# Kernel tuning notes

Measured on AMD Instinct MI355X. Metric: run time of the kernel, lower is better.

The kernel has to match this reference:

```python
import math
import jax, jax.numpy as jnp
import numpy as np

B, L, D, H = 2, 2048, 1024, 16
HD = D // H  # 64

def setup_inputs() -> dict:
    key = jax.random.key(0)
    k1, k2, k3 = jax.random.split(key, 3)
    x = jax.random.normal(k1, (B, L, D), dtype=jnp.float32)
    Wqkv = jax.random.normal(k2, (3 * D, D), dtype=jnp.float32) * (1.0 / math.sqrt(D))
    Wo = jax.random.normal(k3, (D, D), dtype=jnp.float32) * (1.0 / math.sqrt(D))
    return {"x": x, "Wqkv": Wqkv, "Wo": Wo}

def reference(x, Wqkv, Wo):
    # QKV projection (torch Linear: y = x @ W.T), then split
    qkv = jnp.einsum('bld,ed->ble', x, Wqkv)  # [B, L, 3D]
    q, k, v = jnp.split(qkv, 3, axis=-1)
    # [B, H, L, HD]
    q = q.reshape(B, L, H, HD).transpose(0, 2, 1, 3)
    k = k.reshape(B, L, H, HD).transpose(0, 2, 1, 3)
    v = v.reshape(B, L, H, HD).transpose(0, 2, 1, 3)
    # scores; causal mask applied before the 1/sqrt(d) scale (as in source;
    # -inf is unchanged by scaling so math matches scale-then-mask)
    scores = jnp.einsum('bhqd,bhkd->bhqk', q, k)
    causal = jnp.tril(jnp.ones((L, L), dtype=bool))
    scores = jnp.where(causal, scores, -jnp.inf)
    attn = jax.nn.softmax(scores / math.sqrt(HD), axis=-1)
    out = jnp.einsum('bhqk,bhkd->bhqd', attn, v)  # [B, H, L, HD]
    out = out.transpose(0, 2, 1, 3).reshape(B, L, D)
    # output projection (dropout is identity in eval / p=0)
    return jnp.einsum('bld,ed->ble', out, Wo)
```

## Files before the change

### kernel.cpp

```cpp
#include <hip/hip_runtime.h>
#include <hip/hip_bf16.h>
#include <cstdint>
#include <cstddef>

#define B_SZ 2
#define L_SEQ 2048
#define DM 1024
#define NH 16
#define HDIM 64
#define BL (B_SZ * L_SEQ)
#define QKV_N (3 * DM)

typedef __attribute__((ext_vector_type(4))) float f32x4;
typedef __attribute__((ext_vector_type(16))) float f32x16;
typedef __attribute__((ext_vector_type(8))) short bf16x8;
typedef __attribute__((ext_vector_type(4))) unsigned int u32x4;
typedef unsigned short u16;
typedef __attribute__((ext_vector_type(4))) unsigned short u16x4;

__device__ __forceinline__ float bf2f(u16 u) {
  union { unsigned int i; float f; } c; c.i = ((unsigned int)u) << 16; return c.f;
}
__device__ __forceinline__ u16 f2bf(float f) {
  union { float f; unsigned int i; } c; c.f = f;
  unsigned int r = c.i + 0x7fffu + ((c.i >> 16) & 1u);
  return (u16)(r >> 16);
}

__device__ __forceinline__ void gload_lds16(const void* g, void* l) {
  __builtin_amdgcn_global_load_lds(
      (const __attribute__((address_space(1))) void*)g,
      (__attribute__((address_space(3))) void*)l, 16, 0, 0);
}

__device__ __forceinline__ f32x16 mfma32(bf16x8 a, bf16x8 b, f32x16 c) {
  return __builtin_amdgcn_mfma_f32_32x32x16_bf16(a, b, c, 0, 0, 0);
}

__device__ __forceinline__ unsigned cvtpk(float lo, float hi) {
  unsigned r;
  asm("v_cvt_pk_bf16_f32 %0, %1, %2" : "=v"(r) : "v"(lo), "v"(hi));
  return r;
}
__device__ __forceinline__ void plswap(unsigned& a, unsigned& b) {
  asm("v_permlane32_swap_b32 %0, %1" : "+v"(a), "+v"(b));
}

template <int BASE>
__device__ __forceinline__ bf16x8 pack_bfrag(const f32x16& v) {
  unsigned a  = cvtpk(v[BASE + 0], v[BASE + 1]);
  unsigned a2 = cvtpk(v[BASE + 2], v[BASE + 3]);
  unsigned b  = cvtpk(v[BASE + 4], v[BASE + 5]);
  unsigned b2 = cvtpk(v[BASE + 6], v[BASE + 7]);
  plswap(a, b);
  plswap(a2, b2);
  u32x4 fw; fw[0] = a; fw[1] = a2; fw[2] = b; fw[3] = b2;
  return __builtin_bit_cast(bf16x8, fw);
}

__global__ __launch_bounds__(256) void cvt_f32_bf16(const float* __restrict__ in,
                                                    u16* __restrict__ out, int n4) {
  int i = blockIdx.x * blockDim.x + threadIdx.x;
  const int stride = gridDim.x * blockDim.x;
  for (; i < n4; i += stride) {
    float4 v = ((const float4*)in)[i];
    u16x4 o;
    o[0] = f2bf(v.x); o[1] = f2bf(v.y); o[2] = f2bf(v.z); o[3] = f2bf(v.w);
    ((u16x4*)out)[i] = o;
  }
}

template <bool BF16_OUT>
__global__ __launch_bounds__(256) void gemm_bt(
    const u16* __restrict__ A, const u16* __restrict__ B,
    void* __restrict__ Cv, int M, int N, int K) {
  __shared__ u16 As[128 * 32];
  __shared__ u16 Bs[128 * 32];
  const int tid = threadIdx.x;
  const int lane = tid & 63, w = tid >> 6;
  const int lr = lane & 15, lg = lane >> 4;
  const int wr = w >> 1, wc = w & 1;
  const int bm = blockIdx.y * 128, bn = blockIdx.x * 128;

  f32x4 acc[4][4] = {};

  const int l4 = lane >> 2;
  const int csw = ((lane & 3) ^ ((lane >> 3) & 3)) * 8;
  const size_t aoff0 = (size_t)(bm + (w * 2 + 0) * 16 + l4) * K + csw;
  const size_t aoff1 = (size_t)(bm + (w * 2 + 1) * 16 + l4) * K + csw;
  const size_t boff0 = (size_t)(bn + (w * 2 + 0) * 16 + l4) * K + csw;
  const size_t boff1 = (size_t)(bn + (w * 2 + 1) * 16 + l4) * K + csw;
  u16* As0 = As + (w * 2 + 0) * 512;
  u16* As1 = As + (w * 2 + 1) * 512;
  u16* Bs0 = Bs + (w * 2 + 0) * 512;
  u16* Bs1 = Bs + (w * 2 + 1) * 512;
  const int sw_rd = (lr >> 1) & 3;

  for (int k0 = 0; k0 < K; k0 += 32) {
    gload_lds16(A + aoff0 + k0, As0);
    gload_lds16(A + aoff1 + k0, As1);
    gload_lds16(B + boff0 + k0, Bs0);
    gload_lds16(B + boff1 + k0, Bs1);
    __syncthreads();

    bf16x8 af[4], bfr[4];
#pragma unroll
    for (int mt = 0; mt < 4; ++mt) {
      const int row = wr * 64 + mt * 16 + lr;
      af[mt] = *(const bf16x8*)&As[row * 32 + ((lg ^ sw_rd) * 8)];
    }
#pragma unroll
    for (int nt = 0; nt < 4; ++nt) {
      const int row = wc * 64 + nt * 16 + lr;
      bfr[nt] = *(const bf16x8*)&Bs[row * 32 + ((lg ^ sw_rd) * 8)];
    }
#pragma unroll
    for (int mt = 0; mt < 4; ++mt)
#pragma unroll
      for (int nt = 0; nt < 4; ++nt)
        acc[mt][nt] = __builtin_amdgcn_mfma_f32_16x16x32_bf16(af[mt], bfr[nt],
                                                              acc[mt][nt], 0, 0, 0);
    __syncthreads();
  }

#pragma unroll
  for (int mt = 0; mt < 4; ++mt)
#pragma unroll
    for (int nt = 0; nt < 4; ++nt)
#pragma unroll
      for (int r = 0; r < 4; ++r) {
        const int row = bm + wr * 64 + mt * 16 + lg * 4 + r;
        const int col = bn + wc * 64 + nt * 16 + lr;
        if (BF16_OUT)
          ((u16*)Cv)[(size_t)row * N + col] = f2bf(acc[mt][nt][r]);
        else
          ((float*)Cv)[(size_t)row * N + col] = acc[mt][nt][r];
      }
}

__global__ __launch_bounds__(256) void attn_fused(const u16* __restrict__ qkv,
                                                  u16* __restrict__ aout) {
  __shared__ u16 Kl[2][64 * 64];
  __shared__ u16 Vt[2][64 * 64];

  const int tid = threadIdx.x;
  const int lane = tid & 63, w = tid >> 6;
  const int l31 = lane & 31, hi = lane >> 5;
  const int id = (int)blockIdx.x;
  const int bh = id & 31, slot = id >> 5;
  const int qt = slot < 8 ? 15 - 2 * slot : 2 * (slot - 8);
  const int b = bh >> 4, h = bh & 15;
  const u16* base = qkv + (size_t)b * L_SEQ * QKV_N;
  const int W = qt * 128 + w * 32;
  const int nt = 2 * qt + 2;
  const int qrow = W + l31;

  const int krow = tid >> 2;
  const int ks0 = (tid & 3) * 2;
  const int kr7 = krow & 7;
  const int vd0 = (tid & 31) * 2;
  const int vkb = tid >> 5;
  const u16* gpk_base = base + (size_t)krow * QKV_N + DM + h * HDIM + ks0 * 8;
  const u16* gpv_base = base + (size_t)(vkb * 8) * QKV_N + 2 * DM + h * HDIM + vd0;

  bf16x8 kr0, kr1;
  unsigned int vtmp[8];

  auto issue_loads = [&](int t) {
    const u16* gpk = gpk_base + (size_t)t * 64 * QKV_N;
    kr0 = *(const bf16x8*)(gpk);
    kr1 = *(const bf16x8*)(gpk + 8);
    const u16* gpv = gpv_base + (size_t)t * 64 * QKV_N;
#pragma unroll
    for (int j = 0; j < 8; ++j)
      vtmp[j] = *(const unsigned int*)(gpv + (size_t)j * QKV_N);
  };
  auto write_lds = [&](int buf) {
    *(bf16x8*)&Kl[buf][krow * 64 + ((ks0 ^ kr7) * 8)] = kr0;
    *(bf16x8*)&Kl[buf][krow * 64 + (((ks0 + 1) ^ kr7) * 8)] = kr1;
    bf16x8 v0, v1;
#pragma unroll
    for (int j = 0; j < 8; ++j) {
      v0[j] = (short)(vtmp[j] & 0xffffu);
      v1[j] = (short)(vtmp[j] >> 16);
    }
    *(bf16x8*)&Vt[buf][vd0 * 64 + ((vkb ^ (vd0 & 7)) * 8)] = v0;
    *(bf16x8*)&Vt[buf][(vd0 + 1) * 64 + ((vkb ^ ((vd0 + 1) & 7)) * 8)] = v1;
  };

  bf16x8 bq[4];
  {
    const u16* qp = base + (size_t)qrow * QKV_N + h * HDIM + hi * 8;
#pragma unroll
    for (int dc = 0; dc < 4; ++dc) {
      bf16x8 tq = *(const bf16x8*)(qp + dc * 16);
#pragma unroll
      for (int i = 0; i < 8; ++i)
        tq[i] = (short)f2bf(bf2f((u16)tq[i]) * 0.18033688f);
      bq[dc] = tq;
    }
  }

  f32x16 acc0 = {}, acc1 = {};
  float mrow = -1e30f, lrow = 0.f;

  issue_loads(0);
  write_lds(0);
  __syncthreads();

  for (int t = 0; t < nt; ++t) {
    const int cur = t & 1;
    if (t + 1 < nt) issue_loads(t + 1);

    if (64 * t <= W + 31) {
      f32x16 s0 = {}, s1 = {};
      const int lsw = lane & 7;
#pragma unroll
      for (int dc = 0; dc < 4; ++dc) {
        const int sl = ((dc * 2 + hi) ^ lsw) * 8;
        const bf16x8 k0 = *(const bf16x8*)&Kl[cur][l31 * 64 + sl];
        const bf16x8 k1 = *(const bf16x8*)&Kl[cur][(32 + l31) * 64 + sl];
        s0 = mfma32(k0, bq[dc], s0);
        s1 = mfma32(k1, bq[dc], s1);
      }

      if (64 * t + 63 > W) {
#pragma unroll
        for (int r = 0; r < 16; ++r) {
          const int kg = t * 64 + (r & 3) + 8 * (r >> 2) + 4 * hi;
          if (kg > qrow) s0[r] = -1e30f;
          if (kg + 32 > qrow) s1[r] = -1e30f;
        }
      }

      float px = fmaxf(s0[0], s1[0]);
#pragma unroll
      for (int r = 1; r < 16; ++r) px = fmaxf(px, fmaxf(s0[r], s1[r]));
      px = fmaxf(px, __shfl_xor(px, 32));

      if (!__all(px <= mrow + 8.f)) {
        const float mnew = fmaxf(mrow, px);
        const float alpha = exp2f(mrow - mnew);
        mrow = mnew;
        lrow *= alpha;
#pragma unroll
        for (int i = 0; i < 16; ++i) { acc0[i] *= alpha; acc1[i] *= alpha; }
      }

      float rs = 0.f;
#pragma unroll
      for (int r = 0; r < 16; ++r) {
        s0[r] = exp2f(s0[r] - mrow); rs += s0[r];
        s1[r] = exp2f(s1[r] - mrow); rs += s1[r];
      }
      rs += __shfl_xor(rs, 32);
      lrow += rs;

      const bf16x8 pf0 = pack_bfrag<0>(s0);
      const bf16x8 pf1 = pack_bfrag<8>(s0);
      const bf16x8 pf2 = pack_bfrag<0>(s1);
      const bf16x8 pf3 = pack_bfrag<8>(s1);

#pragma unroll
      for (int c = 0; c < 4; ++c) {
        const bf16x8 pf = c == 0 ? pf0 : c == 1 ? pf1 : c == 2 ? pf2 : pf3;
        const int sl = ((c * 2 + hi) ^ lsw) * 8;
        const bf16x8 va = *(const bf16x8*)&Vt[cur][l31 * 64 + sl];
        const bf16x8 vb = *(const bf16x8*)&Vt[cur][(32 + l31) * 64 + sl];
        acc0 = mfma32(va, pf, acc0);
        acc1 = mfma32(vb, pf, acc1);
      }
    }

    if (t + 1 < nt) write_lds((t + 1) & 1);
    __syncthreads();
  }

  const float inv = 1.f / lrow;
#pragma unroll
  for (int i = 0; i < 16; ++i) { acc0[i] *= inv; acc1[i] *= inv; }
  const bf16x8 of0 = pack_bfrag<0>(acc0);
  const bf16x8 of1 = pack_bfrag<8>(acc0);
  const bf16x8 of2 = pack_bfrag<0>(acc1);
  const bf16x8 of3 = pack_bfrag<8>(acc1);
  u16* op = aout + (size_t)(b * L_SEQ + qrow) * DM + h * HDIM + hi * 8;
  *(bf16x8*)(op + 0)  = of0;
  *(bf16x8*)(op + 16) = of1;
  *(bf16x8*)(op + 32) = of2;
  *(bf16x8*)(op + 48) = of3;
}

extern "C" void kernel_launch(void* const* d_in, const int* in_sizes, int n_in,
                              void* d_out, int out_size, void* d_ws, size_t ws_size,
                              hipStream_t stream) {
  (void)in_sizes; (void)n_in; (void)out_size; (void)ws_size;
  const float* x = (const float*)d_in[0];
  const float* wqkv = (const float*)d_in[1];
  const float* wo = (const float*)d_in[2];

  char* ws = (char*)d_ws;
  u16* x_bf = (u16*)(ws);
  u16* w_bf = (u16*)(ws + (size_t)(8u << 20));
  u16* wo_bf = (u16*)(ws + (size_t)(14u << 20));
  u16* qkv_bf = (u16*)(ws + (size_t)(16u << 20));
  u16* ao_bf = x_bf;

  cvt_f32_bf16<<<2048, 256, 0, stream>>>(x, x_bf, BL * DM / 4);
  cvt_f32_bf16<<<2048, 256, 0, stream>>>(wqkv, w_bf, QKV_N * DM / 4);
  cvt_f32_bf16<<<1024, 256, 0, stream>>>(wo, wo_bf, DM * DM / 4);

  dim3 g1(QKV_N / 128, BL / 128);
  gemm_bt<true><<<g1, 256, 0, stream>>>(x_bf, w_bf, (void*)qkv_bf, BL, QKV_N, DM);

  attn_fused<<<dim3(512), 256, 0, stream>>>(qkv_bf, ao_bf);

  dim3 g3(DM / 128, BL / 128);
  gemm_bt<false><<<g3, 256, 0, stream>>>(ao_bf, wo_bf, d_out, BL, DM, DM);
}
```

Baseline: 139.3 us.

## Stage K tiles via direct global-to-LDS loads and repack V with byte permutes

K tiles are now copied straight from global memory into LDS with a gload_lds16 helper, using an XOR-swizzled source address so the LDS layout matches the existing reads. This removes the register round trip and the separate LDS store for K. V transposition now uses v_perm byte permutes to build 128-bit LDS writes under a new swizzle pattern, with the read-side swizzle changed to match. The change also adds s_setprio around the MFMA blocks and turns the max and sum reductions into trees to shorten dependency chains. The new swizzles must agree exactly between writers and readers, otherwise results are silently wrong.

New measurement: 149.9 us. 7.6% more time.

```diff
diff --git a/kernel.cpp b/kernel.cpp
--- a/kernel.cpp
+++ b/kernel.cpp
@@ -155,37 +155,36 @@
   const int nt = 2 * qt + 2;
   const int qrow = W + l31;
 
-  const int krow = tid >> 2;
-  const int ks0 = (tid & 3) * 2;
-  const int kr7 = krow & 7;
+  const u16* kf_src = base + (size_t)(w * 16 + (lane >> 3)) * QKV_N + DM +
+                      h * HDIM + (((lane & 7) ^ (lane >> 3)) * 8);
+  auto stage_K = [&](int t, int buf) {
+    const u16* s = kf_src + (size_t)t * 64 * QKV_N;
+    gload_lds16(s, &Kl[buf][w * 1024]);
+    gload_lds16(s + (size_t)8 * QKV_N, &Kl[buf][w * 1024 + 512]);
+  };
+
   const int vd0 = (tid & 31) * 2;
   const int vkb = tid >> 5;
-  const u16* gpk_base = base + (size_t)krow * QKV_N + DM + h * HDIM + ks0 * 8;
+  const int vge = tid & 7;
+  const int vgo = (tid & 7) ^ 4;
   const u16* gpv_base = base + (size_t)(vkb * 8) * QKV_N + 2 * DM + h * HDIM + vd0;
-
-  bf16x8 kr0, kr1;
   unsigned int vtmp[8];
 
-  auto issue_loads = [&](int t) {
-    const u16* gpk = gpk_base + (size_t)t * 64 * QKV_N;
-    kr0 = *(const bf16x8*)(gpk);
-    kr1 = *(const bf16x8*)(gpk + 8);
+  auto issue_V = [&](int t) {
     const u16* gpv = gpv_base + (size_t)t * 64 * QKV_N;
 #pragma unroll
     for (int j = 0; j < 8; ++j)
       vtmp[j] = *(const unsigned int*)(gpv + (size_t)j * QKV_N);
   };
-  auto write_lds = [&](int buf) {
-    *(bf16x8*)&Kl[buf][krow * 64 + ((ks0 ^ kr7) * 8)] = kr0;
-    *(bf16x8*)&Kl[buf][krow * 64 + (((ks0 + 1) ^ kr7) * 8)] = kr1;
-    bf16x8 v0, v1;
-#pragma unroll
-    for (int j = 0; j < 8; ++j) {
-      v0[j] = (short)(vtmp[j] & 0xffffu);
-      v1[j] = (short)(vtmp[j] >> 16);
-    }
-    *(bf16x8*)&Vt[buf][vd0 * 64 + ((vkb ^ (vd0 & 7)) * 8)] = v0;
-    *(bf16x8*)&Vt[buf][(vd0 + 1) * 64 + ((vkb ^ ((vd0 + 1) & 7)) * 8)] = v1;
+  auto write_V = [&](int buf) {
+    u32x4 lo, hiw;
+#pragma unroll
+    for (int j = 0; j < 4; ++j) {
+      lo[j]  = __builtin_amdgcn_perm(vtmp[2 * j + 1], vtmp[2 * j], 0x05040100u);
+      hiw[j] = __builtin_amdgcn_perm(vtmp[2 * j + 1], vtmp[2 * j], 0x07060302u);
+    }
+    *(u32x4*)&Vt[buf][vd0 * 64 + ((vkb ^ vge) * 8)] = lo;
+    *(u32x4*)&Vt[buf][(vd0 + 1) * 64 + ((vkb ^ vgo) * 8)] = hiw;
   };
 
   bf16x8 bq[4];
@@ -204,17 +203,24 @@
   f32x16 acc0 = {}, acc1 = {};
   float mrow = -1e30f, lrow = 0.f;
 
-  issue_loads(0);
-  write_lds(0);
+  const int vg = ((l31 >> 1) & 7) ^ ((l31 & 1) << 2);
+  const int lsw = l31 & 7;
+
+  stage_K(0, 0);
+  issue_V(0);
+  write_V(0);
   __syncthreads();
 
   for (int t = 0; t < nt; ++t) {
     const int cur = t & 1;
-    if (t + 1 < nt) issue_loads(t + 1);
+    if (t + 1 < nt) {
+      stage_K(t + 1, cur ^ 1);
+      issue_V(t + 1);
+    }
 
     if (64 * t <= W + 31) {
       f32x16 s0 = {}, s1 = {};
-      const int lsw = lane & 7;
+      __builtin_amdgcn_s_setprio(1);
 #pragma unroll
       for (int dc = 0; dc < 4; ++dc) {
         const int sl = ((dc * 2 + hi) ^ lsw) * 8;
@@ -223,6 +229,7 @@
         s0 = mfma32(k0, bq[dc], s0);
         s1 = mfma32(k1, bq[dc], s1);
       }
+      __builtin_amdgcn_s_setprio(0);
 
       if (64 * t + 63 > W) {
 #pragma unroll
@@ -233,9 +240,13 @@
         }
       }
 
-      float px = fmaxf(s0[0], s1[0]);
-#pragma unroll
-      for (int r = 1; r < 16; ++r) px = fmaxf(px, fmaxf(s0[r], s1[r]));
+      float mx[8];
+#pragma unroll
+      for (int i = 0; i < 8; ++i)
+        mx[i] = fmaxf(fmaxf(s0[i], s0[i + 8]), fmaxf(s1[i], s1[i + 8]));
+#pragma unroll
+      for (int i = 0; i < 4; ++i) mx[i] = fmaxf(mx[i], mx[i + 4]);
+      float px = fmaxf(fmaxf(mx[0], mx[2]), fmaxf(mx[1], mx[3]));
       px = fmaxf(px, __shfl_xor(px, 32));
 
       if (!__all(px <= mrow + 8.f)) {
@@ -247,12 +258,18 @@
         for (int i = 0; i < 16; ++i) { acc0[i] *= alpha; acc1[i] *= alpha; }
       }
 
-      float rs = 0.f;
 #pragma unroll
       for (int r = 0; r < 16; ++r) {
-        s0[r] = exp2f(s0[r] - mrow); rs += s0[r];
-        s1[r] = exp2f(s1[r] - mrow); rs += s1[r];
-      }
+        s0[r] = exp2f(s0[r] - mrow);
+        s1[r] = exp2f(s1[r] - mrow);
+      }
+      float sm[8];
+#pragma unroll
+      for (int i = 0; i < 8; ++i)
+        sm[i] = (s0[i] + s0[i + 8]) + (s1[i] + s1[i + 8]);
+#pragma unroll
+      for (int i = 0; i < 4; ++i) sm[i] += sm[i + 4];
+      float rs = (sm[0] + sm[2]) + (sm[1] + sm[3]);
       rs += __shfl_xor(rs, 32);
       lrow += rs;
 
@@ -261,18 +278,20 @@
       const bf16x8 pf2 = pack_bfrag<0>(s1);
       const bf16x8 pf3 = pack_bfrag<8>(s1);
 
+      __builtin_amdgcn_s_setprio(1);
 #pragma unroll
       for (int c = 0; c < 4; ++c) {
         const bf16x8 pf = c == 0 ? pf0 : c == 1 ? pf1 : c == 2 ? pf2 : pf3;
-        const int sl = ((c * 2 + hi) ^ lsw) * 8;
+        const int sl = ((c * 2 + hi) ^ vg) * 8;
         const bf16x8 va = *(const bf16x8*)&Vt[cur][l31 * 64 + sl];
         const bf16x8 vb = *(const bf16x8*)&Vt[cur][(32 + l31) * 64 + sl];
         acc0 = mfma32(va, pf, acc0);
         acc1 = mfma32(vb, pf, acc1);
       }
-    }
-
-    if (t + 1 < nt) write_lds((t + 1) & 1);
+      __builtin_amdgcn_s_setprio(0);
+    }
+
+    if (t + 1 < nt) write_V(cur ^ 1);
     __syncthreads();
   }
 
```

## Double attention KV tile to 128 keys per iteration with chunk-level causal skipping

Applied to the files above, without the earlier changes.

Raises the attention kernel's K/V tile from 64 to 128 keys, which halves the number of loop iterations and the block-wide barriers, and gives each step more MFMA work. Causal skipping now happens per 32-key chunk: on the diagonal tile, chunks past the wave's rows are set to -inf and their QK and PV MFMAs are skipped. The V transpose into LDS is rebuilt with byte-permute packing and a new swizzle for the 128-wide layout. In exchange, LDS use doubles to 64KB, more registers are held for the larger prefetch, and the diagonal tile leaves more waves idle.

New measurement: 163.6 us. +17.4%, slower.

```diff
diff --git a/kernel.cpp b/kernel.cpp
--- a/kernel.cpp
+++ b/kernel.cpp
@@ -56,6 +56,23 @@
   plswap(a2, b2);
   u32x4 fw; fw[0] = a; fw[1] = a2; fw[2] = b; fw[3] = b2;
   return __builtin_bit_cast(bf16x8, fw);
+}
+
+__device__ __forceinline__ float vmax16(const f32x16& v) {
+  float a0 = fmaxf(v[0], v[8]), a1 = fmaxf(v[1], v[9]);
+  float a2 = fmaxf(v[2], v[10]), a3 = fmaxf(v[3], v[11]);
+  float a4 = fmaxf(v[4], v[12]), a5 = fmaxf(v[5], v[13]);
+  float a6 = fmaxf(v[6], v[14]), a7 = fmaxf(v[7], v[15]);
+  a0 = fmaxf(a0, a4); a1 = fmaxf(a1, a5); a2 = fmaxf(a2, a6); a3 = fmaxf(a3, a7);
+  return fmaxf(fmaxf(a0, a2), fmaxf(a1, a3));
+}
+
+__device__ __forceinline__ void maskv(f32x16& v, int hi, int l31) {
+#pragma unroll
+  for (int r = 0; r < 16; ++r) {
+    const int kk = (r & 3) + 8 * (r >> 2) + 4 * hi;
+    if (kk > l31) v[r] = -1e30f;
+  }
 }
 
 __global__ __launch_bounds__(256) void cvt_f32_bf16(const float* __restrict__ in,
@@ -140,8 +157,8 @@
 
 __global__ __launch_bounds__(256) void attn_fused(const u16* __restrict__ qkv,
                                                   u16* __restrict__ aout) {
-  __shared__ u16 Kl[2][64 * 64];
-  __shared__ u16 Vt[2][64 * 64];
+  __shared__ u16 Kl[2][128 * 64];
+  __shared__ u16 Vt[2][64 * 128];
 
   const int tid = threadIdx.x;
   const int lane = tid & 63, w = tid >> 6;
@@ -151,41 +168,47 @@
   const int qt = slot < 8 ? 15 - 2 * slot : 2 * (slot - 8);
   const int b = bh >> 4, h = bh & 15;
   const u16* base = qkv + (size_t)b * L_SEQ * QKV_N;
-  const int W = qt * 128 + w * 32;
-  const int nt = 2 * qt + 2;
-  const int qrow = W + l31;
-
-  const int krow = tid >> 2;
-  const int ks0 = (tid & 3) * 2;
+  const int nt = qt + 1;
+  const int qrow = qt * 128 + w * 32 + l31;
+
+  const int krow = tid >> 1;
+  const int kcb = (tid & 1) * 4;
   const int kr7 = krow & 7;
+  const u16* gpk_base = base + (size_t)krow * QKV_N + DM + h * HDIM + kcb * 8;
+  bf16x8 krg[4];
+
   const int vd0 = (tid & 31) * 2;
   const int vkb = tid >> 5;
-  const u16* gpk_base = base + (size_t)krow * QKV_N + DM + h * HDIM + ks0 * 8;
-  const u16* gpv_base = base + (size_t)(vkb * 8) * QKV_N + 2 * DM + h * HDIM + vd0;
-
-  bf16x8 kr0, kr1;
-  unsigned int vtmp[8];
+  const int vge = tid & 7;
+  const int vgo = (tid & 7) ^ 4;
+  const u16* gpv_base = base + (size_t)(vkb * 16) * QKV_N + 2 * DM + h * HDIM + vd0;
+  unsigned int vtmp[16];
 
   auto issue_loads = [&](int t) {
-    const u16* gpk = gpk_base + (size_t)t * 64 * QKV_N;
-    kr0 = *(const bf16x8*)(gpk);
-    kr1 = *(const bf16x8*)(gpk + 8);
-    const u16* gpv = gpv_base + (size_t)t * 64 * QKV_N;
-#pragma unroll
-    for (int j = 0; j < 8; ++j)
+    const u16* gpk = gpk_base + (size_t)t * 128 * QKV_N;
+#pragma unroll
+    for (int q = 0; q < 4; ++q) krg[q] = *(const bf16x8*)(gpk + q * 8);
+    const u16* gpv = gpv_base + (size_t)t * 128 * QKV_N;
+#pragma unroll
+    for (int j = 0; j < 16; ++j)
       vtmp[j] = *(const unsigned int*)(gpv + (size_t)j * QKV_N);
   };
   auto write_lds = [&](int buf) {
-    *(bf16x8*)&Kl[buf][krow * 64 + ((ks0 ^ kr7) * 8)] = kr0;
-    *(bf16x8*)&Kl[buf][krow * 64 + (((ks0 + 1) ^ kr7) * 8)] = kr1;
-    bf16x8 v0, v1;
-#pragma unroll
-    for (int j = 0; j < 8; ++j) {
-      v0[j] = (short)(vtmp[j] & 0xffffu);
-      v1[j] = (short)(vtmp[j] >> 16);
-    }
-    *(bf16x8*)&Vt[buf][vd0 * 64 + ((vkb ^ (vd0 & 7)) * 8)] = v0;
-    *(bf16x8*)&Vt[buf][(vd0 + 1) * 64 + ((vkb ^ ((vd0 + 1) & 7)) * 8)] = v1;
+#pragma unroll
+    for (int q = 0; q < 4; ++q)
+      *(bf16x8*)&Kl[buf][krow * 64 + (((kcb + q) ^ kr7) * 8)] = krg[q];
+    u32x4 lo0, lo1, hi0, hi1;
+#pragma unroll
+    for (int j = 0; j < 4; ++j) {
+      lo0[j] = __builtin_amdgcn_perm(vtmp[2 * j + 1], vtmp[2 * j], 0x05040100u);
+      hi0[j] = __builtin_amdgcn_perm(vtmp[2 * j + 1], vtmp[2 * j], 0x07060302u);
+      lo1[j] = __builtin_amdgcn_perm(vtmp[2 * j + 9], vtmp[2 * j + 8], 0x05040100u);
+      hi1[j] = __builtin_amdgcn_perm(vtmp[2 * j + 9], vtmp[2 * j + 8], 0x07060302u);
+    }
+    *(u32x4*)&Vt[buf][vd0 * 128 + (((2 * vkb + 0) ^ vge) * 8)] = lo0;
+    *(u32x4*)&Vt[buf][vd0 * 128 + (((2 * vkb + 1) ^ vge) * 8)] = lo1;
+    *(u32x4*)&Vt[buf][(vd0 + 1) * 128 + (((2 * vkb + 0) ^ vgo) * 8)] = hi0;
+    *(u32x4*)&Vt[buf][(vd0 + 1) * 128 + (((2 * vkb + 1) ^ vgo) * 8)] = hi1;
   };
 
   bf16x8 bq[4];
@@ -204,6 +227,9 @@
   f32x16 acc0 = {}, acc1 = {};
   float mrow = -1e30f, lrow = 0.f;
 
+  const int vg = ((l31 >> 1) & 7) ^ ((l31 & 1) << 2);
+  const int lsw = l31 & 7;
+
   issue_loads(0);
   write_lds(0);
   __syncthreads();
@@ -212,67 +238,73 @@
     const int cur = t & 1;
     if (t + 1 < nt) issue_loads(t + 1);
 
-    if (64 * t <= W + 31) {
-      f32x16 s0 = {}, s1 = {};
-      const int lsw = lane & 7;
-#pragma unroll
-      for (int dc = 0; dc < 4; ++dc) {
-        const int sl = ((dc * 2 + hi) ^ lsw) * 8;
-        const bf16x8 k0 = *(const bf16x8*)&Kl[cur][l31 * 64 + sl];
-        const bf16x8 k1 = *(const bf16x8*)&Kl[cur][(32 + l31) * 64 + sl];
-        s0 = mfma32(k0, bq[dc], s0);
-        s1 = mfma32(k1, bq[dc], s1);
-      }
-
-      if (64 * t + 63 > W) {
-#pragma unroll
-        for (int r = 0; r < 16; ++r) {
-          const int kg = t * 64 + (r & 3) + 8 * (r >> 2) + 4 * hi;
-          if (kg > qrow) s0[r] = -1e30f;
-          if (kg + 32 > qrow) s1[r] = -1e30f;
-        }
-      }
-
-      float px = fmaxf(s0[0], s1[0]);
-#pragma unroll
-      for (int r = 1; r < 16; ++r) px = fmaxf(px, fmaxf(s0[r], s1[r]));
-      px = fmaxf(px, __shfl_xor(px, 32));
-
-      if (!__all(px <= mrow + 8.f)) {
-        const float mnew = fmaxf(mrow, px);
-        const float alpha = exp2f(mrow - mnew);
-        mrow = mnew;
-        lrow *= alpha;
-#pragma unroll
-        for (int i = 0; i < 16; ++i) { acc0[i] *= alpha; acc1[i] *= alpha; }
-      }
-
-      float rs = 0.f;
-#pragma unroll
-      for (int r = 0; r < 16; ++r) {
-        s0[r] = exp2f(s0[r] - mrow); rs += s0[r];
-        s1[r] = exp2f(s1[r] - mrow); rs += s1[r];
-      }
-      rs += __shfl_xor(rs, 32);
-      lrow += rs;
-
-      const bf16x8 pf0 = pack_bfrag<0>(s0);
-      const bf16x8 pf1 = pack_bfrag<8>(s0);
-      const bf16x8 pf2 = pack_bfrag<0>(s1);
-      const bf16x8 pf3 = pack_bfrag<8>(s1);
-
-#pragma unroll
-      for (int c = 0; c < 4; ++c) {
-        const bf16x8 pf = c == 0 ? pf0 : c == 1 ? pf1 : c == 2 ? pf2 : pf3;
-        const int sl = ((c * 2 + hi) ^ lsw) * 8;
-        const bf16x8 va = *(const bf16x8*)&Vt[cur][l31 * 64 + sl];
-        const bf16x8 vb = *(const bf16x8*)&Vt[cur][(32 + l31) * 64 + sl];
-        acc0 = mfma32(va, pf, acc0);
-        acc1 = mfma32(vb, pf, acc1);
-      }
-    }
-
-    if (t + 1 < nt) write_lds((t + 1) & 1);
+    f32x16 s0, s1, s2, s3;
+#define QKC(c, sv)                                                             \
+    if (t < qt || (c) <= w) {                                                  \
+      sv = f32x16{};                                                           \
+      _Pragma("unroll")                                                        \
+      for (int dc = 0; dc < 4; ++dc) {                                         \
+        const bf16x8 kk = *(const bf16x8*)                                     \
+            &Kl[cur][((c) * 32 + l31) * 64 + (((dc * 2 + hi) ^ lsw) * 8)];     \
+        sv = mfma32(kk, bq[dc], sv);                                           \
+      }                                                                        \
+    } else {                                                                   \
+      sv = -1e30f;                                                             \
+    }
+    QKC(0, s0) QKC(1, s1) QKC(2, s2) QKC(3, s3)
+#undef QKC
+
+    if (t == qt) {
+      if (w == 0) maskv(s0, hi, l31);
+      else if (w == 1) maskv(s1, hi, l31);
+      else if (w == 2) maskv(s2, hi, l31);
+      else maskv(s3, hi, l31);
+    }
+
+    float px = fmaxf(fmaxf(vmax16(s0), vmax16(s1)), fmaxf(vmax16(s2), vmax16(s3)));
+    px = fmaxf(px, __shfl_xor(px, 32));
+
+    if (!__all(px <= mrow + 8.f)) {
+      const float mnew = fmaxf(mrow, px);
+      const float alpha = exp2f(mrow - mnew);
+      mrow = mnew;
+      lrow *= alpha;
+#pragma unroll
+      for (int i = 0; i < 16; ++i) { acc0[i] *= alpha; acc1[i] *= alpha; }
+    }
+
+    float rs = 0.f;
+#define PVC(c, sv)                                                             \
+    if (t < qt || (c) <= w) {                                                  \
+      float t0 = 0.f, t1 = 0.f;                                                \
+      _Pragma("unroll")                                                        \
+      for (int r = 0; r < 8; ++r) {                                            \
+        sv[r] = exp2f(sv[r] - mrow);  t0 += sv[r];                             \
+        sv[r + 8] = exp2f(sv[r + 8] - mrow); t1 += sv[r + 8];                  \
+      }                                                                        \
+      rs += t0 + t1;                                                           \
+      const bf16x8 pfa = pack_bfrag<0>(sv);                                    \
+      const bf16x8 pfb = pack_bfrag<8>(sv);                                    \
+      {                                                                        \
+        const int sl = ((4 * (c) + hi) ^ vg) * 8;                              \
+        acc0 = mfma32(*(const bf16x8*)&Vt[cur][l31 * 128 + sl], pfa, acc0);    \
+        acc1 = mfma32(*(const bf16x8*)&Vt[cur][(32 + l31) * 128 + sl], pfa,    \
+                      acc1);                                                   \
+      }                                                                        \
+      {                                                                        \
+        const int sl = ((4 * (c) + 2 + hi) ^ vg) * 8;                          \
+        acc0 = mfma32(*(const bf16x8*)&Vt[cur][l31 * 128 + sl], pfb, acc0);    \
+        acc1 = mfma32(*(const bf16x8*)&Vt[cur][(32 + l31) * 128 + sl], pfb,    \
+                      acc1);                                                   \
+      }                                                                        \
+    }
+    PVC(0, s0) PVC(1, s1) PVC(2, s2) PVC(3, s3)
+#undef PVC
+
+    rs += __shfl_xor(rs, 32);
+    lrow += rs;
+
+    if (t + 1 < nt) write_lds(cur ^ 1);
     __syncthreads();
   }
 
```
